# Kernel optimization log

Measured on AMD Instinct MI355X. Metric: run time of the kernel, lower is better.

The kernel has to match this reference:

```python
import jax, jax.numpy as jnp
import numpy as np

B, N, C, CI = 2, 8192, 128, 128
K_SAMP, K_NN = 120, 30  # sampling_ratio, nn_nb
GN_GROUPS, GN_CH = 2, 128
EPS = 1e-5


def setup_inputs() -> dict:
    key = jax.random.key(0)
    ks = jax.random.split(key, 7)
    return {
        "points": jax.random.normal(ks[0], (B, N, 3), jnp.float32),
        "feature": jax.random.normal(ks[1], (B, N, C), jnp.float32),
        "instance_feature": jax.random.normal(ks[2], (B, N, CI), jnp.float32),
        "kpam_w1": jax.random.normal(ks[3], (K_NN, K_NN), jnp.float32) * 0.1,
        "kpam_w2": jax.random.normal(ks[4], (K_NN, K_NN), jnp.float32) * 0.1,
        "conv_w": jax.random.normal(ks[5], (128, 131), jnp.float32) * 0.05,
        "gn_gamma": jnp.ones((GN_CH,), jnp.float32),
        "gn_beta": jnp.zeros((GN_CH,), jnp.float32),
        "mlp_w": jax.random.normal(ks[6], (3, 256), jnp.float32) * 0.05,
        "mlp_b": jnp.zeros((3,), jnp.float32),
    }


def _key_indices(n):
    # replicate torch module: np.random.seed(1234); shuffle(arange(N)); take first 120
    rs = np.random.RandomState(1234)
    l = np.arange(n)
    rs.shuffle(l)
    return jnp.asarray(l[:K_SAMP])


def reference(points, feature, instance_feature, kpam_w1, kpam_w2,
              conv_w, gn_gamma, gn_beta, mlp_w, mlp_b):
    Bv, Nv, _ = points.shape
    idx = _key_indices(Nv)                              # [120] static indices
    key_points = points[:, idx]                         # [B,120,3]
    feat_s = feature[:, idx]                            # [B,120,128]
    inst_s = instance_feature[:, idx]                   # [B,120,CI]

    # cos_dist: -(1 - cos) == cos - 1
    fn = instance_feature / jnp.linalg.norm(instance_feature, axis=-1, keepdims=True)
    gn = inst_s / jnp.linalg.norm(inst_s, axis=-1, keepdims=True)
    dist = jnp.einsum('bnc,bkc->bnk', fn, gn) - 1.0     # [B,N,120]

    topk_dist, topk_idx = jax.lax.top_k(dist, K_NN)     # [B,N,30]

    gather = jax.vmap(lambda tab, ix: tab[ix])          # tab [120,D], ix [N,30]
    topk_kp = gather(key_points, topk_idx)              # [B,N,30,3]
    topk_feat = gather(feat_s, topk_idx)                # [B,N,30,128]

    direction = topk_kp - points[:, :, None, :]         # [B,N,30,3]
    x = jnp.concatenate([topk_feat, direction], axis=3) # [B,N,30,131]

    # KPAM: two 1x1 conv1d over k-channel of topk_dist, softmax over k
    a = jax.nn.relu(jnp.einsum('bnk,ok->bno', topk_dist, kpam_w1))
    a = jnp.einsum('bno,po->bnp', a, kpam_w2)
    attn = jax.nn.softmax(a, axis=2)[..., None]         # [B,N,30,1]
    fa = attn * x                                       # [B,N,30,131]

    # conv1: 1x1 Conv2d 131->128 on layout [B,131,30,N]
    y = jnp.einsum('bnkc,oc->bokn', fa, conv_w)         # [B,128,30,N]

    # GroupNorm(2, 128)
    yg = y.reshape(Bv, GN_GROUPS, GN_CH // GN_GROUPS, K_NN, Nv)
    mu = yg.mean(axis=(2, 3, 4), keepdims=True)
    var = yg.var(axis=(2, 3, 4), keepdims=True)
    yg = (yg - mu) * jax.lax.rsqrt(var + EPS)
    y = yg.reshape(Bv, GN_CH, K_NN, Nv)
    y = y * gn_gamma[None, :, None, None] + gn_beta[None, :, None, None]
    y = jnp.where(y >= 0, y, 0.2 * y)                   # LeakyReLU(0.2)

    y = y.max(axis=2)                                   # max over k -> [B,128,N]
    feat_cat = jnp.concatenate([y, feature.transpose(0, 2, 1)], axis=1)  # [B,256,N]

    offsets = jnp.einsum('bcn,oc->bon', feat_cat, mlp_w) + mlp_b[None, :, None]
    return offsets  # [B,3,N]
```

## Files before the change

kernel.cpp:

```cpp
#include <hip/hip_runtime.h>

#define Bv   2
#define Nv   8192
#define Cv   128
#define KSv  120
#define KNNv 30

namespace mtns {
struct MTState { unsigned mt[624]; int mti; };
constexpr void mt_seed(MTState& s, unsigned seed) {
  for (int pos = 0; pos < 624; ++pos) {
    s.mt[pos] = seed;
    seed = 1812433253u * (seed ^ (seed >> 30)) + (unsigned)pos + 1u;
  }
  s.mti = 624;
}
constexpr unsigned mt_next(MTState& s) {
  if (s.mti >= 624) {
    for (int i = 0; i < 624; ++i) {
      unsigned y = (s.mt[i] & 0x80000000u) | (s.mt[(i + 1) % 624] & 0x7fffffffu);
      unsigned v = s.mt[(i + 397) % 624] ^ (y >> 1);
      s.mt[i] = (y & 1u) ? (v ^ 0x9908b0dfu) : v;
    }
    s.mti = 0;
  }
  unsigned y = s.mt[s.mti++];
  y ^= y >> 11;
  y ^= (y << 7) & 0x9d2c5680u;
  y ^= (y << 15) & 0xefc60000u;
  y ^= y >> 18;
  return y;
}
struct IdxTable { int v[KSv]; };
constexpr IdxTable make_idx() {
  MTState st{};
  mt_seed(st, 1234u);
  int arr[Nv] = {};
  for (int i = 0; i < Nv; ++i) arr[i] = i;
  for (int i = Nv - 1; i > 0; --i) {
    unsigned mask = (unsigned)i;
    mask |= mask >> 1; mask |= mask >> 2; mask |= mask >> 4;
    mask |= mask >> 8; mask |= mask >> 16;
    unsigned j = 0;
    do { j = mt_next(st) & mask; } while (j > (unsigned)i);
    int tmp = arr[i]; arr[i] = arr[(int)j]; arr[(int)j] = tmp;
  }
  IdxTable out{};
  for (int k = 0; k < KSv; ++k) out.v[k] = arr[k];
  return out;
}
}

__constant__ mtns::IdxTable IDX = mtns::make_idx();

__device__ __forceinline__ float wave_sum(float v) {
  #pragma unroll
  for (int m = 32; m; m >>= 1) v += __shfl_xor(v, m);
  return v;
}

__device__ __forceinline__ float opaque(float x) {
  asm volatile("" : "+v"(x));
  return x;
}

__device__ __forceinline__ float npyv_dot(const float4* __restrict__ grow, int sw,
                                          const float4* __restrict__ irow) {
  float4 acc[4];
  acc[0] = float4{0,0,0,0}; acc[1] = float4{0,0,0,0};
  acc[2] = float4{0,0,0,0}; acc[3] = float4{0,0,0,0};
  #pragma unroll 4
  for (int c4 = 0; c4 < 32; ++c4) {
    float4 g = grow[c4 ^ sw];
    float4 f = irow[c4];
    float4& a = acc[c4 & 3];
    a.x = fmaf(g.x, f.x, a.x); a.y = fmaf(g.y, f.y, a.y);
    a.z = fmaf(g.z, f.z, a.z); a.w = fmaf(g.w, f.w, a.w);
  }
  float4 h0, h1, h;
  h0.x = acc[0].x + acc[2].x; h0.y = acc[0].y + acc[2].y;
  h0.z = acc[0].z + acc[2].z; h0.w = acc[0].w + acc[2].w;
  h1.x = acc[1].x + acc[3].x; h1.y = acc[1].y + acc[3].y;
  h1.z = acc[1].z + acc[3].z; h1.w = acc[1].w + acc[3].w;
  h.x = h0.x + h1.x; h.y = h0.y + h1.y; h.z = h0.z + h1.z; h.w = h0.w + h1.w;
  float sx = h.x + h.z;
  float sy = h.y + h.w;
  return sx + sy;
}

__global__ void k0_prepare(const float* __restrict__ points,
                           const float* __restrict__ feature,
                           const float* __restrict__ inst,
                           const float* __restrict__ conv_w,
                           float* __restrict__ gn32W,
                           float* __restrict__ GW) {
  int bk = blockIdx.x;
  int b = bk / KSv, kp = bk % KSv;
  int jg = IDX.v[kp];
  int t = threadIdx.x;
  __shared__ float featS[Cv];
  __shared__ float rowS[Cv];
  __shared__ float ptS[3];
  __shared__ float nAcc[8];
  __shared__ float nrmSh;
  long rowi = (long)b * Nv + jg;
  float iv = inst[rowi * Cv + t];
  rowS[t] = iv;
  featS[t] = feature[rowi * Cv + t];
  if (t < 3) ptS[t] = points[rowi * 3 + t];
  __syncthreads();
  if (t < 8) {
    float x0 = rowS[t];
    float acc = opaque(x0 * x0);
    #pragma unroll
    for (int i = 1; i < 16; ++i) {
      float xv = rowS[8 * i + t];
      acc = acc + opaque(xv * xv);
    }
    nAcc[t] = acc;
  }
  __syncthreads();
  if (t == 0) {
    float res = ((nAcc[0] + nAcc[1]) + (nAcc[2] + nAcc[3])) +
                ((nAcc[4] + nAcc[5]) + (nAcc[6] + nAcc[7]));
    nrmSh = sqrtf(res);
  }
  __syncthreads();
  gn32W[(b * KSv + kp) * Cv + t] = iv / nrmSh;
  const float* cw = conv_w + t * 131;
  float acc = 0.f;
  #pragma unroll 8
  for (int c = 0; c < Cv; ++c) acc = fmaf(featS[c], cw[c], acc);
  acc = fmaf(ptS[0], cw[128], fmaf(ptS[1], cw[129], fmaf(ptS[2], cw[130], acc)));
  GW[(b * KSv + kp) * Cv + t] = acc;
}

__global__ __launch_bounds__(512, 1) void k2_main(
    const float* __restrict__ points,
    const float* __restrict__ inst,
    const float* __restrict__ w1,
    const float* __restrict__ w2,
    const float* __restrict__ conv_w,
    const float* __restrict__ gamma,
    const float* __restrict__ gn32,
    const float* __restrict__ GW,
    float* __restrict__ Msel,
    float2* __restrict__ part) {
  __shared__ float4 gnS[KSv * 32];
  __shared__ float sc[8 * 256];

  int bid = blockIdx.x;
  int b = bid >> 9;
  int chunk = bid & 511;
  int tid = threadIdx.x;
  int w = tid >> 6, l = tid & 63;

  const float4* gnG = (const float4*)(gn32 + (long)b * KSv * Cv);
  for (int i = tid; i < KSv * 32; i += 512) {
    int kp = i >> 5, c4 = i & 31;
    gnS[kp * 32 + (c4 ^ (kp & 31))] = gnG[i];
  }
  __syncthreads();

  float* wb = sc + w * 256;
  float2* fnS2 = (float2*)wb;
  float* distS = wb + 128;
  float* tvp = wb;
  int*   tip = (int*)(wb + 32);
  float* asp = wb + 64;
  float* atp = wb + 96;

  int c0 = 2 * l, c1 = 2 * l + 1;
  float ga0 = gamma[c0], ga1 = gamma[c1];
  float cwa0 = conv_w[c0 * 131 + 128], cwb0 = conv_w[c0 * 131 + 129],
        cwc0 = conv_w[c0 * 131 + 130];
  float cwa1 = conv_w[c1 * 131 + 128], cwb1 = conv_w[c1 * 131 + 129],
        cwc1 = conv_w[c1 * 131 + 130];
  const float* Gb = GW + (long)b * KSv * Cv;
  const float NINF = -__builtin_inff();

  #pragma clang loop unroll(disable)
  for (int e = 0; e < 2; ++e) {
    int n = chunk * 16 + 2 * w + e;
    long row = (long)b * Nv + n;
    __builtin_amdgcn_wave_barrier();
    float2 iv2 = *(const float2*)(inst + row * Cv + c0);
    fnS2[l] = iv2;
    float p0 = points[row * 3 + 0];
    float p1 = points[row * 3 + 1];
    float p2 = points[row * 3 + 2];
    __builtin_amdgcn_wave_barrier();
    float acc = 0.f;
    if (l < 8) {
      float x0 = wb[l];
      acc = opaque(x0 * x0);
      #pragma unroll
      for (int i = 1; i < 16; ++i) {
        float xv = wb[8 * i + l];
        acc = acc + opaque(xv * xv);
      }
    }
    float r0 = __shfl(acc, 0), r1 = __shfl(acc, 1), r2 = __shfl(acc, 2),
          r3 = __shfl(acc, 3), r4 = __shfl(acc, 4), r5 = __shfl(acc, 5),
          r6 = __shfl(acc, 6), r7 = __shfl(acc, 7);
    float nrm = sqrtf(((r0 + r1) + (r2 + r3)) + ((r4 + r5) + (r6 + r7)));
    __builtin_amdgcn_wave_barrier();
    float2 fn2;
    fn2.x = iv2.x / nrm;
    fn2.y = iv2.y / nrm;
    fnS2[l] = fn2;
    __builtin_amdgcn_wave_barrier();
    const float4* irow = (const float4*)wb;
    float d0 = npyv_dot(gnS + l * 32, l & 31, irow) - 1.0f;
    float d1 = NINF;
    if (l < 56) d1 = npyv_dot(gnS + (64 + l) * 32, l & 31, irow) - 1.0f;
    distS[l] = d0;
    if (l < 56) distS[64 + l] = d1;
    __builtin_amdgcn_wave_barrier();
    int rk0 = 0, rk1 = 0;
    const float4* dv = (const float4*)distS;
    int t1 = 64 + l;
    #pragma unroll 6
    for (int j4 = 0; j4 < KSv / 4; ++j4) {
      float4 w4 = dv[j4];
      int base = j4 * 4;
      rk0 += (w4.x > d0) || (w4.x == d0 && (base + 0) < l);
      rk0 += (w4.y > d0) || (w4.y == d0 && (base + 1) < l);
      rk0 += (w4.z > d0) || (w4.z == d0 && (base + 2) < l);
      rk0 += (w4.w > d0) || (w4.w == d0 && (base + 3) < l);
      rk1 += (w4.x > d1) || (w4.x == d1 && (base + 0) < t1);
      rk1 += (w4.y > d1) || (w4.y == d1 && (base + 1) < t1);
      rk1 += (w4.z > d1) || (w4.z == d1 && (base + 2) < t1);
      rk1 += (w4.w > d1) || (w4.w == d1 && (base + 3) < t1);
    }
    if (rk0 < KNNv) { tvp[rk0] = d0; tip[rk0] = l; }
    if (l < 56 && rk1 < KNNv) { tvp[rk1] = d1; tip[rk1] = t1; }
    __builtin_amdgcn_wave_barrier();
    if (l < KNNv) {
      float a = 0.f;
      #pragma unroll
      for (int k = 0; k < KNNv; ++k) a = fmaf(tvp[k], w1[l * KNNv + k], a);
      asp[l] = fmaxf(a, 0.f);
    }
    __builtin_amdgcn_wave_barrier();
    float a2 = NINF;
    if (l < KNNv) {
      float s2 = 0.f;
      #pragma unroll
      for (int o = 0; o < KNNv; ++o) s2 = fmaf(asp[o], w2[l * KNNv + o], s2);
      a2 = s2;
    }
    float m = a2;
    #pragma unroll
    for (int msk = 32; msk; msk >>= 1) m = fmaxf(m, __shfl_xor(m, msk));
    float ev = (l < KNNv) ? __expf(a2 - m) : 0.f;
    float ssum = wave_sum(ev);
    float inv = 1.0f / ssum;
    if (l < KNNv) atp[l] = ev * inv;
    __builtin_amdgcn_wave_barrier();
    float pw0 = fmaf(p0, cwa0, fmaf(p1, cwb0, p2 * cwc0));
    float pw1 = fmaf(p0, cwa1, fmaf(p1, cwb1, p2 * cwc1));
    float mx0 = NINF, mn0 = -NINF, mx1 = NINF, mn1 = -NINF;
    float s = 0.f, q = 0.f;
    #pragma unroll 6
    for (int k = 0; k < KNNv; ++k) {
      float ak = atp[k];
      int jk = tip[k];
      float2 g = *(const float2*)(Gb + jk * Cv + c0);
      float y0 = ak * (g.x - pw0);
      float y1 = ak * (g.y - pw1);
      mx0 = fmaxf(mx0, y0); mn0 = fminf(mn0, y0);
      mx1 = fmaxf(mx1, y1); mn1 = fminf(mn1, y1);
      s += y0 + y1;
      q = fmaf(y0, y0, fmaf(y1, y1, q));
    }
    float2 msel;
    msel.x = (ga0 >= 0.f) ? mx0 : mn0;
    msel.y = (ga1 >= 0.f) ? mx1 : mn1;
    *(float2*)(Msel + row * Cv + c0) = msel;
    float sg = s, qg = q;
    #pragma unroll
    for (int msk = 16; msk; msk >>= 1) {
      sg += __shfl_xor(sg, msk);
      qg += __shfl_xor(qg, msk);
    }
    if ((l & 31) == 0) part[row * 2 + (l >> 5)] = make_float2(sg, qg);
  }
}

__global__ void k3_stats(const float2* __restrict__ part,
                         float2* __restrict__ stats) {
  int bg = blockIdx.x;
  int b = bg >> 1, g = bg & 1;
  int tid = threadIdx.x;
  __shared__ double sd[256], qd[256];
  double s = 0, q = 0;
  for (int i = tid; i < Nv; i += 256) {
    float2 p = part[((long)b * Nv + i) * 2 + g];
    s += p.x;
    q += p.y;
  }
  sd[tid] = s; qd[tid] = q;
  __syncthreads();
  for (int st = 128; st > 0; st >>= 1) {
    if (tid < st) { sd[tid] += sd[tid + st]; qd[tid] += qd[tid + st]; }
    __syncthreads();
  }
  if (tid == 0) {
    const double cnt = 64.0 * 30.0 * 8192.0;
    double mu = sd[0] / cnt;
    double var = qd[0] / cnt - mu * mu;
    double rs = 1.0 / sqrt(var + 1e-5);
    stats[bg] = make_float2((float)mu, (float)rs);
  }
}

__global__ __launch_bounds__(256) void k4_out(
    const float* __restrict__ feature,
    const float* __restrict__ gamma,
    const float* __restrict__ beta,
    const float* __restrict__ mlp_w,
    const float* __restrict__ mlp_b,
    const float* __restrict__ Msel,
    const float2* __restrict__ stats,
    float* __restrict__ out) {
  int rr = threadIdx.x >> 7;
  int t = threadIdx.x & 127;
  long row = (long)blockIdx.x * 2 + rr;
  int b = (int)(row >> 13), n = (int)(row & (Nv - 1));
  int g = t >> 6;
  float2 st = stats[b * 2 + g];
  float gam = gamma[t], bet = beta[t];
  float M = Msel[row * Cv + t];
  float yv = fmaf((M - st.x) * st.y, gam, bet);
  yv = (yv >= 0.f) ? yv : 0.2f * yv;
  float fv = feature[row * Cv + t];
  float o0 = yv * mlp_w[0 * 256 + t] + fv * mlp_w[0 * 256 + 128 + t];
  float o1 = yv * mlp_w[1 * 256 + t] + fv * mlp_w[1 * 256 + 128 + t];
  float o2 = yv * mlp_w[2 * 256 + t] + fv * mlp_w[2 * 256 + 128 + t];
  o0 = wave_sum(o0);
  o1 = wave_sum(o1);
  o2 = wave_sum(o2);
  __shared__ float red[2][2][3];
  if ((t & 63) == 0) {
    red[rr][t >> 6][0] = o0; red[rr][t >> 6][1] = o1; red[rr][t >> 6][2] = o2;
  }
  __syncthreads();
  if (t < 3)
    out[(long)b * 3 * Nv + (long)t * Nv + n] =
        red[rr][0][t] + red[rr][1][t] + mlp_b[t];
}

extern "C" void kernel_launch(void* const* d_in, const int* in_sizes, int n_in,
                              void* d_out, int out_size, void* d_ws, size_t ws_size,
                              hipStream_t stream) {
  const float* points  = (const float*)d_in[0];
  const float* feature = (const float*)d_in[1];
  const float* inst    = (const float*)d_in[2];
  const float* w1      = (const float*)d_in[3];
  const float* w2      = (const float*)d_in[4];
  const float* conv_w  = (const float*)d_in[5];
  const float* gamma   = (const float*)d_in[6];
  const float* beta    = (const float*)d_in[7];
  const float* mlp_w   = (const float*)d_in[8];
  const float* mlp_b   = (const float*)d_in[9];
  float* out = (float*)d_out;

  char* ws = (char*)d_ws;
  float* gn32  = (float*)(ws);
  float* GW    = (float*)(ws + 122880);
  float* Msel  = (float*)(ws + 245760);
  float2* part = (float2*)(ws + 245760 + 8388608);
  float2* stats= (float2*)(ws + 245760 + 8388608 + 262144);

  k0_prepare<<<dim3(Bv * KSv), dim3(128), 0, stream>>>(points, feature, inst,
                                                       conv_w, gn32, GW);
  k2_main<<<dim3(1024), dim3(512), 0, stream>>>(points, inst, w1, w2, conv_w,
                                                gamma, gn32, GW, Msel, part);
  k3_stats<<<dim3(4), dim3(256), 0, stream>>>(part, stats);
  k4_out<<<dim3(Bv * Nv / 2), dim3(256), 0, stream>>>(feature, gamma, beta,
                                                      mlp_w, mlp_b, Msel,
                                                      stats, out);
}
```

Before: 177.0 us.

## Process two rows per wave jointly, fuse GroupNorm stats reduction via last-block atomic

Each wave now handles its two points together instead of looping: the distance dot products share loads of key-feature rows from LDS across both rows, and the rank, KPAM and gather loops are interleaved for two rows. Top-k values and attention weights stay in registers and are broadcast with readlane instead of LDS round trips. Per-block partial sums are reduced in LDS, and the last block, found with an atomic counter, computes the GroupNorm statistics, which removes the separate stats kernel launch. The launch bounds hint is raised for occupancy, at the cost of higher register pressure and a serialized tail in the last block.

```diff
diff --git a/kernel.cpp b/kernel.cpp
--- a/kernel.cpp
+++ b/kernel.cpp
@@ -64,24 +64,19 @@
   return x;
 }
 
-__device__ __forceinline__ float npyv_dot(const float4* __restrict__ grow, int sw,
-                                          const float4* __restrict__ irow) {
-  float4 acc[4];
-  acc[0] = float4{0,0,0,0}; acc[1] = float4{0,0,0,0};
-  acc[2] = float4{0,0,0,0}; acc[3] = float4{0,0,0,0};
-  #pragma unroll 4
-  for (int c4 = 0; c4 < 32; ++c4) {
-    float4 g = grow[c4 ^ sw];
-    float4 f = irow[c4];
-    float4& a = acc[c4 & 3];
-    a.x = fmaf(g.x, f.x, a.x); a.y = fmaf(g.y, f.y, a.y);
-    a.z = fmaf(g.z, f.z, a.z); a.w = fmaf(g.w, f.w, a.w);
-  }
+__device__ __forceinline__ float rdf(float v, int k) {
+  return __int_as_float(__builtin_amdgcn_readlane(__float_as_int(v), k));
+}
+__device__ __forceinline__ int rdi(int v, int k) {
+  return __builtin_amdgcn_readlane(v, k);
+}
+
+__device__ __forceinline__ float npyv_reduce(const float4* a) {
   float4 h0, h1, h;
-  h0.x = acc[0].x + acc[2].x; h0.y = acc[0].y + acc[2].y;
-  h0.z = acc[0].z + acc[2].z; h0.w = acc[0].w + acc[2].w;
-  h1.x = acc[1].x + acc[3].x; h1.y = acc[1].y + acc[3].y;
-  h1.z = acc[1].z + acc[3].z; h1.w = acc[1].w + acc[3].w;
+  h0.x = a[0].x + a[2].x; h0.y = a[0].y + a[2].y;
+  h0.z = a[0].z + a[2].z; h0.w = a[0].w + a[2].w;
+  h1.x = a[1].x + a[3].x; h1.y = a[1].y + a[3].y;
+  h1.z = a[1].z + a[3].z; h1.w = a[1].w + a[3].w;
   h.x = h0.x + h1.x; h.y = h0.y + h1.y; h.z = h0.z + h1.z; h.w = h0.w + h1.w;
   float sx = h.x + h.z;
   float sy = h.y + h.w;
@@ -93,11 +88,13 @@
                            const float* __restrict__ inst,
                            const float* __restrict__ conv_w,
                            float* __restrict__ gn32W,
-                           float* __restrict__ GW) {
+                           float* __restrict__ GW,
+                           int* __restrict__ counter) {
   int bk = blockIdx.x;
   int b = bk / KSv, kp = bk % KSv;
   int jg = IDX.v[kp];
   int t = threadIdx.x;
+  if (bk == 0 && t == 0) *counter = 0;
   __shared__ float featS[Cv];
   __shared__ float rowS[Cv];
   __shared__ float ptS[3];
@@ -135,7 +132,7 @@
   GW[(b * KSv + kp) * Cv + t] = acc;
 }
 
-__global__ __launch_bounds__(512, 1) void k2_main(
+__global__ __launch_bounds__(512, 4) void k2_main(
     const float* __restrict__ points,
     const float* __restrict__ inst,
     const float* __restrict__ w1,
@@ -145,9 +142,13 @@
     const float* __restrict__ gn32,
     const float* __restrict__ GW,
     float* __restrict__ Msel,
-    float2* __restrict__ part) {
+    float2* __restrict__ part,
+    int* __restrict__ counter,
+    float2* __restrict__ stats) {
   __shared__ float4 gnS[KSv * 32];
-  __shared__ float sc[8 * 256];
+  __shared__ float sc[8 * 512];
+  __shared__ float2 partS[16];
+  __shared__ int lastFlag;
 
   int bid = blockIdx.x;
   int b = bid >> 9;
@@ -162,156 +163,256 @@
   }
   __syncthreads();
 
-  float* wb = sc + w * 256;
-  float2* fnS2 = (float2*)wb;
-  float* distS = wb + 128;
-  float* tvp = wb;
-  int*   tip = (int*)(wb + 32);
-  float* asp = wb + 64;
-  float* atp = wb + 96;
-
-  int c0 = 2 * l, c1 = 2 * l + 1;
-  float ga0 = gamma[c0], ga1 = gamma[c1];
+  float* wb = sc + w * 512;
+  float* fnA = wb;
+  float* fnB = wb + 128;
+  float* dsA = wb + 256;
+  float* dsB = wb + 384;
+  float* tvA = dsA; int* tiA = (int*)(dsA + 32);
+  float* tvB = dsB; int* tiB = (int*)(dsB + 32);
+
+  int c0 = 2 * l;
+  int nA = chunk * 16 + 2 * w;
+  long rowA = (long)b * Nv + nA;
+  long rowB = rowA + 1;
+  const float* Gb = GW + (long)b * KSv * Cv;
+  const float NINF = -__builtin_inff();
+
+  float2 ivA = *(const float2*)(inst + rowA * Cv + c0);
+  float2 ivB = *(const float2*)(inst + rowB * Cv + c0);
+  ((float2*)fnA)[l] = ivA;
+  ((float2*)fnB)[l] = ivB;
+  __builtin_amdgcn_wave_barrier();
+
+  float acc = 0.f;
+  if (l < 16) {
+    const float* xr = (l < 8) ? fnA : fnB;
+    int j = l & 7;
+    float x0 = xr[j];
+    acc = opaque(x0 * x0);
+    #pragma unroll
+    for (int i = 1; i < 16; ++i) {
+      float xv = xr[8 * i + j];
+      acc = acc + opaque(xv * xv);
+    }
+  }
+  float nrmA = sqrtf(((rdf(acc, 0) + rdf(acc, 1)) + (rdf(acc, 2) + rdf(acc, 3))) +
+                     ((rdf(acc, 4) + rdf(acc, 5)) + (rdf(acc, 6) + rdf(acc, 7))));
+  float nrmB = sqrtf(((rdf(acc, 8) + rdf(acc, 9)) + (rdf(acc, 10) + rdf(acc, 11))) +
+                     ((rdf(acc, 12) + rdf(acc, 13)) + (rdf(acc, 14) + rdf(acc, 15))));
+  __builtin_amdgcn_wave_barrier();
+  float2 fA2, fB2;
+  fA2.x = ivA.x / nrmA; fA2.y = ivA.y / nrmA;
+  fB2.x = ivB.x / nrmB; fB2.y = ivB.y / nrmB;
+  ((float2*)fnA)[l] = fA2;
+  ((float2*)fnB)[l] = fB2;
+  __builtin_amdgcn_wave_barrier();
+
+  const float4* fA4 = (const float4*)fnA;
+  const float4* fB4 = (const float4*)fnB;
+  int sw = l & 31;
+  const float4* g0r = gnS + l * 32;
+  int r1 = 64 + l; if (r1 > KSv - 1) r1 = KSv - 1;
+  const float4* g1r = gnS + r1 * 32;
+  float4 aA0[4], aA1[4], aB0[4], aB1[4];
+  #pragma unroll
+  for (int i = 0; i < 4; ++i) {
+    aA0[i] = float4{0,0,0,0}; aA1[i] = float4{0,0,0,0};
+    aB0[i] = float4{0,0,0,0}; aB1[i] = float4{0,0,0,0};
+  }
+  #pragma unroll 4
+  for (int c4 = 0; c4 < 32; ++c4) {
+    float4 fa = fA4[c4];
+    float4 fb = fB4[c4];
+    float4 g0 = g0r[c4 ^ sw];
+    float4 g1 = g1r[c4 ^ sw];
+    int m = c4 & 3;
+    aA0[m].x = fmaf(g0.x, fa.x, aA0[m].x); aA0[m].y = fmaf(g0.y, fa.y, aA0[m].y);
+    aA0[m].z = fmaf(g0.z, fa.z, aA0[m].z); aA0[m].w = fmaf(g0.w, fa.w, aA0[m].w);
+    aB0[m].x = fmaf(g0.x, fb.x, aB0[m].x); aB0[m].y = fmaf(g0.y, fb.y, aB0[m].y);
+    aB0[m].z = fmaf(g0.z, fb.z, aB0[m].z); aB0[m].w = fmaf(g0.w, fb.w, aB0[m].w);
+    aA1[m].x = fmaf(g1.x, fa.x, aA1[m].x); aA1[m].y = fmaf(g1.y, fa.y, aA1[m].y);
+    aA1[m].z = fmaf(g1.z, fa.z, aA1[m].z); aA1[m].w = fmaf(g1.w, fa.w, aA1[m].w);
+    aB1[m].x = fmaf(g1.x, fb.x, aB1[m].x); aB1[m].y = fmaf(g1.y, fb.y, aB1[m].y);
+    aB1[m].z = fmaf(g1.z, fb.z, aB1[m].z); aB1[m].w = fmaf(g1.w, fb.w, aB1[m].w);
+  }
+  float d0A = npyv_reduce(aA0) - 1.0f;
+  float d1A = npyv_reduce(aA1) - 1.0f;
+  float d0B = npyv_reduce(aB0) - 1.0f;
+  float d1B = npyv_reduce(aB1) - 1.0f;
+
+  dsA[l] = d0A;
+  dsB[l] = d0B;
+  if (l < 56) { dsA[64 + l] = d1A; dsB[64 + l] = d1B; }
+  __builtin_amdgcn_wave_barrier();
+
+  float d1Ar = (l < 56) ? d1A : NINF;
+  float d1Br = (l < 56) ? d1B : NINF;
+  int rk0A = 0, rk1A = 0, rk0B = 0, rk1B = 0;
+  const float4* dvA = (const float4*)dsA;
+  const float4* dvB = (const float4*)dsB;
+  int t1 = 64 + l;
+  #pragma unroll 5
+  for (int j4 = 0; j4 < KSv / 4; ++j4) {
+    float4 wA = dvA[j4];
+    float4 wB = dvB[j4];
+    int base = j4 * 4;
+    rk0A += (wA.x > d0A) || (wA.x == d0A && (base + 0) < l);
+    rk0A += (wA.y > d0A) || (wA.y == d0A && (base + 1) < l);
+    rk0A += (wA.z > d0A) || (wA.z == d0A && (base + 2) < l);
+    rk0A += (wA.w > d0A) || (wA.w == d0A && (base + 3) < l);
+    rk1A += (wA.x > d1Ar) || (wA.x == d1Ar && (base + 0) < t1);
+    rk1A += (wA.y > d1Ar) || (wA.y == d1Ar && (base + 1) < t1);
+    rk1A += (wA.z > d1Ar) || (wA.z == d1Ar && (base + 2) < t1);
+    rk1A += (wA.w > d1Ar) || (wA.w == d1Ar && (base + 3) < t1);
+    rk0B += (wB.x > d0B) || (wB.x == d0B && (base + 0) < l);
+    rk0B += (wB.y > d0B) || (wB.y == d0B && (base + 1) < l);
+    rk0B += (wB.z > d0B) || (wB.z == d0B && (base + 2) < l);
+    rk0B += (wB.w > d0B) || (wB.w == d0B && (base + 3) < l);
+    rk1B += (wB.x > d1Br) || (wB.x == d1Br && (base + 0) < t1);
+    rk1B += (wB.y > d1Br) || (wB.y == d1Br && (base + 1) < t1);
+    rk1B += (wB.z > d1Br) || (wB.z == d1Br && (base + 2) < t1);
+    rk1B += (wB.w > d1Br) || (wB.w == d1Br && (base + 3) < t1);
+  }
+  __builtin_amdgcn_wave_barrier();
+  if (rk0A < KNNv) { tvA[rk0A] = d0A; tiA[rk0A] = l; }
+  if (l < 56 && rk1A < KNNv) { tvA[rk1A] = d1A; tiA[rk1A] = t1; }
+  if (rk0B < KNNv) { tvB[rk0B] = d0B; tiB[rk0B] = l; }
+  if (l < 56 && rk1B < KNNv) { tvB[rk1B] = d1B; tiB[rk1B] = t1; }
+  __builtin_amdgcn_wave_barrier();
+  float mytvA = 0.f, mytvB = 0.f;
+  int mytiA = 0, mytiB = 0;
+  if (l < KNNv) {
+    mytvA = tvA[l]; mytiA = tiA[l];
+    mytvB = tvB[l]; mytiB = tiB[l];
+  }
+
+  float aA = 0.f, aB = 0.f;
+  if (l < KNNv) {
+    const float* w1r = w1 + l * KNNv;
+    #pragma unroll 6
+    for (int k = 0; k < KNNv; ++k) {
+      float w1k = w1r[k];
+      aA = fmaf(rdf(mytvA, k), w1k, aA);
+      aB = fmaf(rdf(mytvB, k), w1k, aB);
+    }
+    aA = fmaxf(aA, 0.f);
+    aB = fmaxf(aB, 0.f);
+  }
+  float a2A = NINF, a2B = NINF;
+  if (l < KNNv) {
+    const float* w2r = w2 + l * KNNv;
+    float sA2 = 0.f, sB2 = 0.f;
+    #pragma unroll 6
+    for (int o = 0; o < KNNv; ++o) {
+      float w2o = w2r[o];
+      sA2 = fmaf(rdf(aA, o), w2o, sA2);
+      sB2 = fmaf(rdf(aB, o), w2o, sB2);
+    }
+    a2A = sA2; a2B = sB2;
+  }
+
+  float mA = a2A, mB = a2B;
+  #pragma unroll
+  for (int msk = 32; msk; msk >>= 1) {
+    mA = fmaxf(mA, __shfl_xor(mA, msk));
+    mB = fmaxf(mB, __shfl_xor(mB, msk));
+  }
+  float evA = (l < KNNv) ? __expf(a2A - mA) : 0.f;
+  float evB = (l < KNNv) ? __expf(a2B - mB) : 0.f;
+  float invA = 1.0f / wave_sum(evA);
+  float invB = 1.0f / wave_sum(evB);
+  float atpA = evA * invA;
+  float atpB = evB * invB;
+
+  float pA0 = points[rowA * 3 + 0], pA1 = points[rowA * 3 + 1],
+        pA2 = points[rowA * 3 + 2];
+  float pB0 = points[rowB * 3 + 0], pB1 = points[rowB * 3 + 1],
+        pB2 = points[rowB * 3 + 2];
+  int c1 = c0 + 1;
   float cwa0 = conv_w[c0 * 131 + 128], cwb0 = conv_w[c0 * 131 + 129],
         cwc0 = conv_w[c0 * 131 + 130];
   float cwa1 = conv_w[c1 * 131 + 128], cwb1 = conv_w[c1 * 131 + 129],
         cwc1 = conv_w[c1 * 131 + 130];
-  const float* Gb = GW + (long)b * KSv * Cv;
-  const float NINF = -__builtin_inff();
-
-  #pragma clang loop unroll(disable)
-  for (int e = 0; e < 2; ++e) {
-    int n = chunk * 16 + 2 * w + e;
-    long row = (long)b * Nv + n;
-    __builtin_amdgcn_wave_barrier();
-    float2 iv2 = *(const float2*)(inst + row * Cv + c0);
-    fnS2[l] = iv2;
-    float p0 = points[row * 3 + 0];
-    float p1 = points[row * 3 + 1];
-    float p2 = points[row * 3 + 2];
-    __builtin_amdgcn_wave_barrier();
-    float acc = 0.f;
-    if (l < 8) {
-      float x0 = wb[l];
-      acc = opaque(x0 * x0);
-      #pragma unroll
-      for (int i = 1; i < 16; ++i) {
-        float xv = wb[8 * i + l];
-        acc = acc + opaque(xv * xv);
-      }
-    }
-    float r0 = __shfl(acc, 0), r1 = __shfl(acc, 1), r2 = __shfl(acc, 2),
-          r3 = __shfl(acc, 3), r4 = __shfl(acc, 4), r5 = __shfl(acc, 5),
-          r6 = __shfl(acc, 6), r7 = __shfl(acc, 7);
-    float nrm = sqrtf(((r0 + r1) + (r2 + r3)) + ((r4 + r5) + (r6 + r7)));
-    __builtin_amdgcn_wave_barrier();
-    float2 fn2;
-    fn2.x = iv2.x / nrm;
-    fn2.y = iv2.y / nrm;
-    fnS2[l] = fn2;
-    __builtin_amdgcn_wave_barrier();
-    const float4* irow = (const float4*)wb;
-    float d0 = npyv_dot(gnS + l * 32, l & 31, irow) - 1.0f;
-    float d1 = NINF;
-    if (l < 56) d1 = npyv_dot(gnS + (64 + l) * 32, l & 31, irow) - 1.0f;
-    distS[l] = d0;
-    if (l < 56) distS[64 + l] = d1;
-    __builtin_amdgcn_wave_barrier();
-    int rk0 = 0, rk1 = 0;
-    const float4* dv = (const float4*)distS;
-    int t1 = 64 + l;
-    #pragma unroll 6
-    for (int j4 = 0; j4 < KSv / 4; ++j4) {
-      float4 w4 = dv[j4];
-      int base = j4 * 4;
-      rk0 += (w4.x > d0) || (w4.x == d0 && (base + 0) < l);
-      rk0 += (w4.y > d0) || (w4.y == d0 && (base + 1) < l);
-      rk0 += (w4.z > d0) || (w4.z == d0 && (base + 2) < l);
-      rk0 += (w4.w > d0) || (w4.w == d0 && (base + 3) < l);
-      rk1 += (w4.x > d1) || (w4.x == d1 && (base + 0) < t1);
-      rk1 += (w4.y > d1) || (w4.y == d1 && (base + 1) < t1);
-      rk1 += (w4.z > d1) || (w4.z == d1 && (base + 2) < t1);
-      rk1 += (w4.w > d1) || (w4.w == d1 && (base + 3) < t1);
-    }
-    if (rk0 < KNNv) { tvp[rk0] = d0; tip[rk0] = l; }
-    if (l < 56 && rk1 < KNNv) { tvp[rk1] = d1; tip[rk1] = t1; }
-    __builtin_amdgcn_wave_barrier();
-    if (l < KNNv) {
-      float a = 0.f;
-      #pragma unroll
-      for (int k = 0; k < KNNv; ++k) a = fmaf(tvp[k], w1[l * KNNv + k], a);
-      asp[l] = fmaxf(a, 0.f);
-    }
-    __builtin_amdgcn_wave_barrier();
-    float a2 = NINF;
-    if (l < KNNv) {
-      float s2 = 0.f;
-      #pragma unroll
-      for (int o = 0; o < KNNv; ++o) s2 = fmaf(asp[o], w2[l * KNNv + o], s2);
-      a2 = s2;
-    }
-    float m = a2;
+  float pwA0 = fmaf(pA0, cwa0, fmaf(pA1, cwb0, pA2 * cwc0));
+  float pwA1 = fmaf(pA0, cwa1, fmaf(pA1, cwb1, pA2 * cwc1));
+  float pwB0 = fmaf(pB0, cwa0, fmaf(pB1, cwb0, pB2 * cwc0));
+  float pwB1 = fmaf(pB0, cwa1, fmaf(pB1, cwb1, pB2 * cwc1));
+  float mxA0 = NINF, mnA0 = -NINF, mxA1 = NINF, mnA1 = -NINF;
+  float mxB0 = NINF, mnB0 = -NINF, mxB1 = NINF, mnB1 = -NINF;
+  float sA = 0.f, qA = 0.f, sB = 0.f, qB = 0.f;
+  #pragma unroll 5
+  for (int k = 0; k < KNNv; ++k) {
+    float akA = rdf(atpA, k);
+    float akB = rdf(atpB, k);
+    int jkA = rdi(mytiA, k);
+    int jkB = rdi(mytiB, k);
+    float2 gA = *(const float2*)(Gb + jkA * Cv + c0);
+    float2 gB = *(const float2*)(Gb + jkB * Cv + c0);
+    float yA0 = akA * (gA.x - pwA0);
+    float yA1 = akA * (gA.y - pwA1);
+    float yB0 = akB * (gB.x - pwB0);
+    float yB1 = akB * (gB.y - pwB1);
+    mxA0 = fmaxf(mxA0, yA0); mnA0 = fminf(mnA0, yA0);
+    mxA1 = fmaxf(mxA1, yA1); mnA1 = fminf(mnA1, yA1);
+    mxB0 = fmaxf(mxB0, yB0); mnB0 = fminf(mnB0, yB0);
+    mxB1 = fmaxf(mxB1, yB1); mnB1 = fminf(mnB1, yB1);
+    sA += yA0 + yA1;
+    qA = fmaf(yA0, yA0, fmaf(yA1, yA1, qA));
+    sB += yB0 + yB1;
+    qB = fmaf(yB0, yB0, fmaf(yB1, yB1, qB));
+  }
+  float ga0 = gamma[c0], ga1 = gamma[c1];
+  float2 mselA, mselB;
+  mselA.x = (ga0 >= 0.f) ? mxA0 : mnA0;
+  mselA.y = (ga1 >= 0.f) ? mxA1 : mnA1;
+  mselB.x = (ga0 >= 0.f) ? mxB0 : mnB0;
+  mselB.y = (ga1 >= 0.f) ? mxB1 : mnB1;
+  *(float2*)(Msel + rowA * Cv + c0) = mselA;
+  *(float2*)(Msel + rowB * Cv + c0) = mselB;
+
+  float sg = sA + sB, qg = qA + qB;
+  #pragma unroll
+  for (int msk = 16; msk; msk >>= 1) {
+    sg += __shfl_xor(sg, msk);
+    qg += __shfl_xor(qg, msk);
+  }
+  if ((l & 31) == 0) partS[w * 2 + (l >> 5)] = make_float2(sg, qg);
+  __syncthreads();
+  if (tid == 0) {
+    float s0 = 0.f, q0 = 0.f, s1 = 0.f, q1 = 0.f;
     #pragma unroll
-    for (int msk = 32; msk; msk >>= 1) m = fmaxf(m, __shfl_xor(m, msk));
-    float ev = (l < KNNv) ? __expf(a2 - m) : 0.f;
-    float ssum = wave_sum(ev);
-    float inv = 1.0f / ssum;
-    if (l < KNNv) atp[l] = ev * inv;
-    __builtin_amdgcn_wave_barrier();
-    float pw0 = fmaf(p0, cwa0, fmaf(p1, cwb0, p2 * cwc0));
-    float pw1 = fmaf(p0, cwa1, fmaf(p1, cwb1, p2 * cwc1));
-    float mx0 = NINF, mn0 = -NINF, mx1 = NINF, mn1 = -NINF;
-    float s = 0.f, q = 0.f;
-    #pragma unroll 6
-    for (int k = 0; k < KNNv; ++k) {
-      float ak = atp[k];
-      int jk = tip[k];
-      float2 g = *(const float2*)(Gb + jk * Cv + c0);
-      float y0 = ak * (g.x - pw0);
-      float y1 = ak * (g.y - pw1);
-      mx0 = fmaxf(mx0, y0); mn0 = fminf(mn0, y0);
-      mx1 = fmaxf(mx1, y1); mn1 = fminf(mn1, y1);
-      s += y0 + y1;
-      q = fmaf(y0, y0, fmaf(y1, y1, q));
-    }
-    float2 msel;
-    msel.x = (ga0 >= 0.f) ? mx0 : mn0;
-    msel.y = (ga1 >= 0.f) ? mx1 : mn1;
-    *(float2*)(Msel + row * Cv + c0) = msel;
-    float sg = s, qg = q;
+    for (int wv = 0; wv < 8; ++wv) {
+      s0 += partS[wv * 2].x;     q0 += partS[wv * 2].y;
+      s1 += partS[wv * 2 + 1].x; q1 += partS[wv * 2 + 1].y;
+    }
+    part[bid * 2 + 0] = make_float2(s0, q0);
+    part[bid * 2 + 1] = make_float2(s1, q1);
+    __threadfence();
+    int old = atomicAdd(counter, 1);
+    lastFlag = (old == (int)gridDim.x - 1);
+  }
+  __syncthreads();
+  if (lastFlag && w < 4) {
+    int bb = w >> 1, g = w & 1;
+    double s = 0.0, q = 0.0;
     #pragma unroll
-    for (int msk = 16; msk; msk >>= 1) {
-      sg += __shfl_xor(sg, msk);
-      qg += __shfl_xor(qg, msk);
-    }
-    if ((l & 31) == 0) part[row * 2 + (l >> 5)] = make_float2(sg, qg);
-  }
-}
-
-__global__ void k3_stats(const float2* __restrict__ part,
-                         float2* __restrict__ stats) {
-  int bg = blockIdx.x;
-  int b = bg >> 1, g = bg & 1;
-  int tid = threadIdx.x;
-  __shared__ double sd[256], qd[256];
-  double s = 0, q = 0;
-  for (int i = tid; i < Nv; i += 256) {
-    float2 p = part[((long)b * Nv + i) * 2 + g];
-    s += p.x;
-    q += p.y;
-  }
-  sd[tid] = s; qd[tid] = q;
-  __syncthreads();
-  for (int st = 128; st > 0; st >>= 1) {
-    if (tid < st) { sd[tid] += sd[tid + st]; qd[tid] += qd[tid + st]; }
-    __syncthreads();
-  }
-  if (tid == 0) {
-    const double cnt = 64.0 * 30.0 * 8192.0;
-    double mu = sd[0] / cnt;
-    double var = qd[0] / cnt - mu * mu;
-    double rs = 1.0 / sqrt(var + 1e-5);
-    stats[bg] = make_float2((float)mu, (float)rs);
+    for (int i = 0; i < 8; ++i) {
+      float2 p = part[(bb * 512 + l + 64 * i) * 2 + g];
+      s += (double)p.x;
+      q += (double)p.y;
+    }
+    #pragma unroll
+    for (int msk = 32; msk; msk >>= 1) {
+      s += __shfl_xor(s, msk);
+      q += __shfl_xor(q, msk);
+    }
+    if (l == 0) {
+      const double cnt = 64.0 * 30.0 * 8192.0;
+      double mu = s / cnt;
+      double var = q / cnt - mu * mu;
+      stats[bb * 2 + g] = make_float2((float)mu, (float)(1.0 / sqrt(var + 1e-5)));
+    }
   }
 }
 
@@ -367,17 +468,18 @@
   float* out = (float*)d_out;
 
   char* ws = (char*)d_ws;
-  float* gn32  = (float*)(ws);
-  float* GW    = (float*)(ws + 122880);
-  float* Msel  = (float*)(ws + 245760);
-  float2* part = (float2*)(ws + 245760 + 8388608);
-  float2* stats= (float2*)(ws + 245760 + 8388608 + 262144);
+  float* gn32   = (float*)(ws);
+  float* GW     = (float*)(ws + 122880);
+  float* Msel   = (float*)(ws + 245760);
+  float2* part  = (float2*)(ws + 8634368);
+  int* counter  = (int*)(ws + 8650752);
+  float2* stats = (float2*)(ws + 8650816);
 
   k0_prepare<<<dim3(Bv * KSv), dim3(128), 0, stream>>>(points, feature, inst,
-                                                       conv_w, gn32, GW);
+                                                       conv_w, gn32, GW, counter);
   k2_main<<<dim3(1024), dim3(512), 0, stream>>>(points, inst, w1, w2, conv_w,
-                                                gamma, gn32, GW, Msel, part);
-  k3_stats<<<dim3(4), dim3(256), 0, stream>>>(part, stats);
+                                                gamma, gn32, GW, Msel, part,
+                                                counter, stats);
   k4_out<<<dim3(Bv * Nv / 2), dim3(256), 0, stream>>>(feature, gamma, beta,
                                                       mlp_w, mlp_b, Msel,
                                                       stats, out);
```

Result: faster. 172.9 us (-2.3%).
